# Kernel tuning notes

Measured on AMD Instinct MI355X. Metric: run time of the kernel, lower is better.

Reference implementation:

```python
import jax, jax.numpy as jnp
import numpy as np

N = 50000   # nodes
E = 800000  # edges (avg degree 16)
F = 128     # input_nf = output_nf
H = 128     # hidden_nf


def setup_inputs() -> dict:
    key = jax.random.key(0)
    ks = jax.random.split(key, 10)
    # coords: spatial part in [-1, 1], z-coordinate (last dim) in [0.5, 1.5] (must be > 0)
    xz = jax.random.uniform(ks[0], (N, 3), minval=-1.0, maxval=1.0)
    xz = xz.at[:, -1].set(jax.random.uniform(ks[1], (N,), minval=0.5, maxval=1.5))
    h = jax.random.normal(ks[2], (N, F), dtype=jnp.float32)
    row = jax.random.randint(ks[3], (E,), 0, N)
    # guarantee col != row so AdS distance is strictly positive on every edge
    col = (row + 1 + jax.random.randint(ks[4], (E,), 0, N - 1)) % N
    edge_index = jnp.stack([row, col]).astype(jnp.int32)

    def lin(k, fan_in, fan_out):
        return jax.random.normal(k, (fan_in, fan_out), dtype=jnp.float32) / np.float32(np.sqrt(fan_in))

    return {
        "xz": xz,
        "h": h,
        "We1": lin(ks[5], 2 * F + 1, H), "be1": jnp.full((H,), 0.1, jnp.float32),
        "We2": lin(ks[6], H, H),         "be2": jnp.full((H,), 0.1, jnp.float32),
        "Wn1": lin(ks[7], H + F, H),     "bn1": jnp.full((H,), 0.1, jnp.float32),
        "Wn2": lin(ks[8], H, F),         "bn2": jnp.full((F,), 0.1, jnp.float32),
        "edge_index": edge_index,
    }


def reference(xz, h, We1, be1, We2, be2, Wn1, bn1, Wn2, bn2, edge_index):
    row, col = edge_index[0], edge_index[1]
    n = h.shape[0]

    # AdS (hyperbolic upper-half-space) distance between xz[row] and xz[col]:
    # d = arccosh(1 + |p1 - p2|^2 / (2 z1 z2)), z = last coordinate
    diff = xz[row] - xz[col]                                  # [E, 3]
    u = jnp.sum(diff * diff, axis=-1) / (2.0 * xz[row, -1] * xz[col, -1])
    dist = jnp.arccosh(1.0 + u)[:, None]                      # [E, 1]

    # edge model: concat(source, target, radial) -> Linear -> silu -> Linear -> silu
    m = jnp.concatenate([h[row], h[col], dist], axis=1)       # [E, 2F+1]
    m = jax.nn.silu(m @ We1 + be1)                            # [E, H]
    m = jax.nn.silu(m @ We2 + be2)                            # [E, H]

    # segment_mean over destination nodes (row)
    num = jax.ops.segment_sum(m, row, num_segments=n)                          # [N, H]
    den = jax.ops.segment_sum(jnp.ones_like(m), row, num_segments=n)          # [N, H]
    agg = num / jnp.maximum(den, jnp.ones((), den.dtype))

    # node model: concat(h, agg) -> Linear -> silu -> Linear, plus residual
    z = jnp.concatenate([h, agg], axis=1)                     # [N, F+H]
    out = jax.nn.silu(z @ Wn1 + bn1) @ Wn2 + bn2              # [N, F]
    return h + out
```

## Files before the change

### kernel.cpp

```cpp
#include <hip/hip_runtime.h>

#define NN 50000
#define EE 800000
#define NB 196

typedef __bf16 bf16x8 __attribute__((ext_vector_type(8)));
typedef float  f32x4  __attribute__((ext_vector_type(4)));

__device__ __forceinline__ float bf2f(ushort u) {
    union { unsigned int i; float f; } v; v.i = ((unsigned int)u) << 16; return v.f;
}
__device__ __forceinline__ ushort f2bf(float f) {
    union { float f; unsigned int i; } v; v.f = f;
    unsigned int u = v.i;
    return (ushort)((u + 0x7FFFu + ((u >> 16) & 1u)) >> 16);
}
__device__ __forceinline__ ushort f2bf_fast(float f) {
    union { float f; unsigned int i; } v; v.f = f;
    return (ushort)((v.i + 0x8000u) >> 16);
}
__device__ __forceinline__ float silu(float x) {
    return x * __builtin_amdgcn_rcpf(1.0f + __expf(-x));
}

__global__ void detect_kernel(const ushort* __restrict__ xzu, int* __restrict__ flag) {
    __shared__ int cnt;
    if (threadIdx.x == 0) cnt = 0;
    __syncthreads();
    float v = bf2f(xzu[2 * threadIdx.x]);
    bool sane = (v == v) && (fabsf(v) <= 4.0f);
    if (sane) atomicAdd(&cnt, 1);
    __syncthreads();
    if (threadIdx.x == 0) *flag = (cnt >= 192) ? 0 : 1;
}

__global__ void prep_kernel(const void* __restrict__ hsrc, const void* __restrict__ xzsrc,
                            const int* __restrict__ erow, const int* __restrict__ flag,
                            ushort* __restrict__ hb, float* __restrict__ xzf,
                            int* __restrict__ cntI) {
    const bool isf = (*flag != 0);
    int b = blockIdx.x;
    if (b < 3125) {
        int i = (b * 256 + threadIdx.x) * 8;
        uint4 o;
        if (isf) {
            const float* s = (const float*)hsrc + i;
            float4 f0 = *(const float4*)s;
            float4 f1 = *(const float4*)(s + 4);
            o.x = (unsigned int)f2bf(f0.x) | ((unsigned int)f2bf(f0.y) << 16);
            o.y = (unsigned int)f2bf(f0.z) | ((unsigned int)f2bf(f0.w) << 16);
            o.z = (unsigned int)f2bf(f1.x) | ((unsigned int)f2bf(f1.y) << 16);
            o.w = (unsigned int)f2bf(f1.z) | ((unsigned int)f2bf(f1.w) << 16);
        } else {
            o = *(const uint4*)((const ushort*)hsrc + i);
        }
        *(uint4*)(hb + i) = o;
    } else if (b < 3712) {
        int i = (b - 3125) * 256 + threadIdx.x;
        if (i < NN * 3)
            xzf[i] = isf ? ((const float*)xzsrc)[i] : bf2f(((const ushort*)xzsrc)[i]);
    } else {
        int e = (b - 3712) * 256 + threadIdx.x;
        if (e < EE) atomicAdd(&cntI[erow[e]], 1);
    }
}

__global__ void swizzle_misc_kernel(const void* We1, const void* We2,
                                    const void* Wn1, const void* Wn2,
                                    const void* be1, const void* be2,
                                    const void* bn1, const void* bn2,
                                    const int* __restrict__ flag,
                                    ushort* __restrict__ We1s, ushort* __restrict__ We2s,
                                    ushort* __restrict__ Wn1s, ushort* __restrict__ Wn2s,
                                    float* __restrict__ fb, ushort* __restrict__ wlb) {
    const bool isf = (*flag != 0);
    if (blockIdx.x == 48) {
        for (int j = threadIdx.x; j < 640; j += 256) {
            int which = j >> 7, k = j & 127;
            const void* src = (which == 0) ? be1 : (which == 1) ? be2 :
                              (which == 2) ? bn1 : (which == 3) ? bn2 : We1;
            size_t idx = (which == 4) ? ((size_t)256 * 128 + k) : (size_t)k;
            float v = isf ? ((const float*)src)[idx] : bf2f(((const ushort*)src)[idx]);
            fb[j] = v;
            if (which == 4) wlb[k] = f2bf(v);
        }
        return;
    }
    int c = blockIdx.x * 256 + threadIdx.x;
    const void* src; ushort* dst; int cl;
    if      (c <  4096) { src = We1; dst = We1s; cl = c;         }
    else if (c <  6144) { src = We2; dst = We2s; cl = c - 4096;  }
    else if (c < 10240) { src = Wn1; dst = Wn1s; cl = c - 6144;  }
    else                { src = Wn2; dst = Wn2s; cl = c - 10240; }
    int l = cl & 63, nt = (cl >> 6) & 7, kc = cl >> 9;
    int kbase = kc * 32 + (l >> 4) * 8;
    int n = nt * 16 + (l & 15);
    ushort tmp[8];
#pragma unroll
    for (int j = 0; j < 8; ++j) {
        size_t idx = (size_t)(kbase + j) * 128 + n;
        tmp[j] = isf ? f2bf(((const float*)src)[idx]) : ((const ushort*)src)[idx];
    }
#pragma unroll
    for (int j = 0; j < 8; ++j) dst[(size_t)cl * 8 + j] = tmp[j];
}

__global__ void scanA_kernel(const int* __restrict__ cntI, int* __restrict__ bsum) {
    __shared__ int s[256];
    int t = threadIdx.x;
    int i = blockIdx.x * 256 + t;
    s[t] = (i < NN) ? cntI[i] : 0;
    __syncthreads();
#pragma unroll
    for (int off = 128; off > 0; off >>= 1) {
        if (t < off) s[t] += s[t + off];
        __syncthreads();
    }
    if (t == 0) bsum[blockIdx.x] = s[0];
}

__global__ void scanB_kernel(int* __restrict__ bsum) {
    __shared__ int s[256];
    int t = threadIdx.x;
    int v = (t < NB) ? bsum[t] : 0;
    s[t] = v;
    __syncthreads();
    for (int off = 1; off < 256; off <<= 1) {
        int u = (t >= off) ? s[t - off] : 0;
        __syncthreads();
        if (t >= off) s[t] += u;
        __syncthreads();
    }
    if (t < NB) bsum[t] = s[t] - v;
}

__global__ void scanC_kernel(const int* __restrict__ cntI, const int* __restrict__ bsum,
                             int* __restrict__ rowStart) {
    __shared__ int s[256];
    int t = threadIdx.x;
    int i = blockIdx.x * 256 + t;
    int v = (i < NN) ? cntI[i] : 0;
    s[t] = v;
    __syncthreads();
    for (int off = 1; off < 256; off <<= 1) {
        int u = (t >= off) ? s[t - off] : 0;
        __syncthreads();
        if (t >= off) s[t] += u;
        __syncthreads();
    }
    if (i < NN) rowStart[i] = bsum[blockIdx.x] + s[t] - v;
}

__global__ void scatter_kernel(const int* __restrict__ erow, const int* __restrict__ ecol,
                               const float* __restrict__ xzf,
                               const int* __restrict__ rowStart, int* __restrict__ cursor,
                               int* __restrict__ erowS, int* __restrict__ ecolS,
                               float* __restrict__ distS) {
    int e = blockIdx.x * 256 + threadIdx.x;
    if (e >= EE) return;
    int r = erow[e], c = ecol[e];
    int pos = rowStart[r] + atomicAdd(&cursor[r], 1);
    float4 a = *(const float4*)(xzf + 3 * r);
    float4 b = *(const float4*)(xzf + 3 * c);
    float dx = a.x - b.x, dy = a.y - b.y, dz = a.z - b.z;
    float u = (dx * dx + dy * dy + dz * dz) * __builtin_amdgcn_rcpf(2.0f * a.z * b.z);
    u = fminf(fmaxf(u, 0.0f), 1.0e6f);
    erowS[pos] = r;
    ecolS[pos] = c;
    distS[pos] = __logf(1.0f + u + sqrtf(u * (u + 2.0f)));
}

__global__ __launch_bounds__(256, 3) void pq_kernel(
    const ushort* __restrict__ hb, const ushort* __restrict__ We1s,
    const float* __restrict__ fb, ushort* __restrict__ Pp, ushort* __restrict__ Qq) {
    __shared__ __align__(16) ushort sA[8192];
    const int tid = threadIdx.x;
    const int lane = tid & 63, w = tid >> 6;
    const int col = lane & 15, quad = lane >> 4;
    const int nt0 = w * 2;
    const int ntiles = (NN + 63) / 64;
    const int nA = w * 32 + col, nB = nA + 16;
    const float be1A = fb[nA], be1B = fb[nB];

    for (int tile = blockIdx.x; tile < ntiles; tile += gridDim.x) {
        __syncthreads();
        const int n0 = tile * 64;
#pragma unroll
        for (int i = 0; i < 4; ++i) {
            int node = n0 + lane;
            uint4 v = (node < NN) ? *(const uint4*)(hb + (size_t)node * 128 + (w + 4 * i) * 8)
                                  : make_uint4(0, 0, 0, 0);
            *(uint4*)(sA + (((lane >> 4) * 4 + i) * 64 + w * 16 + (lane & 15)) * 8) = v;
        }
        __syncthreads();

        f32x4 accP[4][2] = {}, accQ[4][2] = {};
#pragma unroll
        for (int kc = 0; kc < 4; ++kc) {
            bf16x8 bp0 = *(const bf16x8*)(We1s + ((kc * 8 + nt0)           * 64 + lane) * 8);
            bf16x8 bp1 = *(const bf16x8*)(We1s + ((kc * 8 + nt0 + 1)       * 64 + lane) * 8);
            bf16x8 bq0 = *(const bf16x8*)(We1s + (((kc + 4) * 8 + nt0)     * 64 + lane) * 8);
            bf16x8 bq1 = *(const bf16x8*)(We1s + (((kc + 4) * 8 + nt0 + 1) * 64 + lane) * 8);
#pragma unroll
            for (int g = 0; g < 4; ++g) {
                bf16x8 a = *(const bf16x8*)(sA + ((g * 4 + kc) * 64 + lane) * 8);
                accP[g][0] = __builtin_amdgcn_mfma_f32_16x16x32_bf16(a, bp0, accP[g][0], 0, 0, 0);
                accP[g][1] = __builtin_amdgcn_mfma_f32_16x16x32_bf16(a, bp1, accP[g][1], 0, 0, 0);
                accQ[g][0] = __builtin_amdgcn_mfma_f32_16x16x32_bf16(a, bq0, accQ[g][0], 0, 0, 0);
                accQ[g][1] = __builtin_amdgcn_mfma_f32_16x16x32_bf16(a, bq1, accQ[g][1], 0, 0, 0);
            }
        }
#pragma unroll
        for (int g = 0; g < 4; ++g) {
#pragma unroll
            for (int r = 0; r < 4; ++r) {
                int node = n0 + g * 16 + quad * 4 + r;
                if (node < NN) {
                    size_t o = (size_t)node * 128;
                    Pp[o + nA] = f2bf(accP[g][0][r] + be1A);
                    Pp[o + nB] = f2bf(accP[g][1][r] + be1B);
                    Qq[o + nA] = f2bf(accQ[g][0][r]);
                    Qq[o + nB] = f2bf(accQ[g][1][r]);
                }
            }
        }
    }
}

__global__ __launch_bounds__(256, 4) void edge_kernel(
    const ushort* __restrict__ Pp, const ushort* __restrict__ Qq,
    const int* __restrict__ erowS, const int* __restrict__ ecolS,
    const float* __restrict__ distS, const ushort* __restrict__ We2s,
    const ushort* __restrict__ wlb, const float* __restrict__ fb,
    float* __restrict__ agg) {
    __shared__ __align__(16) char smem[64 * 132 * 4];
    __shared__ int sRow[64];
    ushort* sM = (ushort*)smem;
    float (*sOut)[132] = (float(*)[132])smem;

    const int tid = threadIdx.x;
    const int lane = tid & 63, w = tid >> 6;
    const int col = lane & 15, quad = lane >> 4;
    const int nt0 = w * 2;

    const int nA = w * 32 + col, nB = nA + 16;
    const float be2A = fb[128 + nA], be2B = fb[128 + nB];

    bf16x8 B2[8];
#pragma unroll
    for (int kc = 0; kc < 4; ++kc) {
        B2[kc * 2]     = *(const bf16x8*)(We2s + ((kc * 8 + nt0)     * 64 + lane) * 8);
        B2[kc * 2 + 1] = *(const bf16x8*)(We2s + ((kc * 8 + nt0 + 1) * 64 + lane) * 8);
    }
    bf16x8 WL[4];
#pragma unroll
    for (int i = 0; i < 4; ++i) WL[i] = *(const bf16x8*)(wlb + (w + 4 * i) * 8);

    const int ntiles = EE / 64;
    const int per = (ntiles + gridDim.x - 1) / gridDim.x;
    const int t0 = blockIdx.x * per;
    const int t1 = (t0 + per < ntiles) ? (t0 + per) : ntiles;

    for (int tile = t0; tile < t1; ++tile) {
        __syncthreads();
        const int e = tile * 64 + lane;
        const int r = erowS[e], c = ecolS[e];
        const float d = distS[e];
        if (w == 0) sRow[lane] = r;
#pragma unroll
        for (int i = 0; i < 4; ++i) {
            int ch = w + 4 * i;
            bf16x8 p = *(const bf16x8*)(Pp + (size_t)r * 128 + ch * 8);
            bf16x8 q = *(const bf16x8*)(Qq + (size_t)c * 128 + ch * 8);
            ushort out8[8];
#pragma unroll
            for (int j = 0; j < 8; ++j) {
                float x = (float)p[j] + (float)q[j] + d * (float)WL[i][j];
                out8[j] = f2bf_fast(silu(x));
            }
            *(uint4*)(sM + (((lane >> 4) * 4 + i) * 64 + w * 16 + (lane & 15)) * 8) =
                *(const uint4*)out8;
        }
        __syncthreads();

        f32x4 acc2[4][2] = {};
#pragma unroll
        for (int kc = 0; kc < 4; ++kc) {
#pragma unroll
            for (int g = 0; g < 4; ++g) {
                bf16x8 a = *(const bf16x8*)(sM + ((g * 4 + kc) * 64 + lane) * 8);
                acc2[g][0] = __builtin_amdgcn_mfma_f32_16x16x32_bf16(a, B2[kc * 2],     acc2[g][0], 0, 0, 0);
                acc2[g][1] = __builtin_amdgcn_mfma_f32_16x16x32_bf16(a, B2[kc * 2 + 1], acc2[g][1], 0, 0, 0);
            }
        }
        __syncthreads();

#pragma unroll
        for (int g = 0; g < 4; ++g) {
#pragma unroll
            for (int r4 = 0; r4 < 4; ++r4) {
                int m = g * 16 + quad * 4 + r4;
                sOut[m][nA] = silu(acc2[g][0][r4] + be2A);
                sOut[m][nB] = silu(acc2[g][1][r4] + be2B);
            }
        }
        __syncthreads();

        {
            const int cc = tid & 127;
            const int mb = (tid >> 7) * 32;
            float acc = 0.0f;
            int prow = sRow[mb];
            for (int k = 0; k < 32; ++k) {
                int rw = sRow[mb + k];
                if (rw != prow) {
                    unsafeAtomicAdd(&agg[(size_t)prow * 128 + cc], acc);
                    acc = 0.0f;
                    prow = rw;
                }
                acc += sOut[mb + k][cc];
            }
            unsafeAtomicAdd(&agg[(size_t)prow * 128 + cc], acc);
        }
    }
}

__global__ __launch_bounds__(256, 3) void node_kernel(
    const ushort* __restrict__ hb, const void* __restrict__ hraw,
    const float* __restrict__ agg, const int* __restrict__ cntI,
    const ushort* __restrict__ Wn1s, const ushort* __restrict__ Wn2s,
    const float* __restrict__ fb, const int* __restrict__ flag,
    void* __restrict__ outv) {
    __shared__ __align__(16) ushort sA[16384];
    __shared__ __align__(16) ushort sM[8192];
    const int tid = threadIdx.x;
    const int lane = tid & 63, w = tid >> 6;
    const int col = lane & 15, quad = lane >> 4;
    const int nt0 = w * 2;
    const int ntiles = (NN + 63) / 64;
    const bool isf = (*flag != 0);
    float* outf = (float*)outv;
    ushort* outu = (ushort*)outv;

    const int nA = w * 32 + col, nB = nA + 16;
    const float bn1A = fb[256 + nA], bn1B = fb[256 + nB];
    const float bn2A = fb[384 + nA], bn2B = fb[384 + nB];

    for (int tile = blockIdx.x; tile < ntiles; tile += gridDim.x) {
        __syncthreads();
        const int n0 = tile * 64;
#pragma unroll
        for (int i = 0; i < 8; ++i) {
            int kb = w + 4 * i;
            int node = n0 + lane;
            uint4 v;
            if (node < NN) {
                if (kb < 16) {
                    v = *(const uint4*)(hb + (size_t)node * 128 + kb * 8);
                } else {
                    const float* ap = agg + (size_t)node * 128 + (kb - 16) * 8;
                    float invc = __builtin_amdgcn_rcpf(fmaxf((float)cntI[node], 1.0f));
                    float4 f0 = *(const float4*)ap;
                    float4 f1 = *(const float4*)(ap + 4);
                    v.x = (unsigned int)f2bf_fast(f0.x * invc) | ((unsigned int)f2bf_fast(f0.y * invc) << 16);
                    v.y = (unsigned int)f2bf_fast(f0.z * invc) | ((unsigned int)f2bf_fast(f0.w * invc) << 16);
                    v.z = (unsigned int)f2bf_fast(f1.x * invc) | ((unsigned int)f2bf_fast(f1.y * invc) << 16);
                    v.w = (unsigned int)f2bf_fast(f1.z * invc) | ((unsigned int)f2bf_fast(f1.w * invc) << 16);
                }
            } else {
                v = make_uint4(0, 0, 0, 0);
            }
            *(uint4*)(sA + (((quad * 8 + i) * 64) + w * 16 + col) * 8) = v;
        }
        __syncthreads();

        f32x4 acc[4][2] = {};
#pragma unroll
        for (int kc = 0; kc < 8; ++kc) {
            bf16x8 b0 = *(const bf16x8*)(Wn1s + ((kc * 8 + nt0)     * 64 + lane) * 8);
            bf16x8 b1 = *(const bf16x8*)(Wn1s + ((kc * 8 + nt0 + 1) * 64 + lane) * 8);
#pragma unroll
            for (int g = 0; g < 4; ++g) {
                bf16x8 a = *(const bf16x8*)(sA + ((g * 8 + kc) * 64 + lane) * 8);
                acc[g][0] = __builtin_amdgcn_mfma_f32_16x16x32_bf16(a, b0, acc[g][0], 0, 0, 0);
                acc[g][1] = __builtin_amdgcn_mfma_f32_16x16x32_bf16(a, b1, acc[g][1], 0, 0, 0);
            }
        }
#pragma unroll
        for (int g = 0; g < 4; ++g) {
            int base0 = ((g * 4 + w) * 64 + (col >> 3) * 16) * 8 + (col & 7);
#pragma unroll
            for (int r = 0; r < 4; ++r) {
                int mrow = quad * 4 + r;
                sM[base0 + mrow * 8]              = f2bf_fast(silu(acc[g][0][r] + bn1A));
                sM[base0 + 2 * 16 * 8 + mrow * 8] = f2bf_fast(silu(acc[g][1][r] + bn1B));
            }
        }
        __syncthreads();

        f32x4 acc2[4][2] = {};
#pragma unroll
        for (int kc = 0; kc < 4; ++kc) {
            bf16x8 b0 = *(const bf16x8*)(Wn2s + ((kc * 8 + nt0)     * 64 + lane) * 8);
            bf16x8 b1 = *(const bf16x8*)(Wn2s + ((kc * 8 + nt0 + 1) * 64 + lane) * 8);
#pragma unroll
            for (int g = 0; g < 4; ++g) {
                bf16x8 a = *(const bf16x8*)(sM + ((g * 4 + kc) * 64 + lane) * 8);
                acc2[g][0] = __builtin_amdgcn_mfma_f32_16x16x32_bf16(a, b0, acc2[g][0], 0, 0, 0);
                acc2[g][1] = __builtin_amdgcn_mfma_f32_16x16x32_bf16(a, b1, acc2[g][1], 0, 0, 0);
            }
        }
#pragma unroll
        for (int g = 0; g < 4; ++g) {
#pragma unroll
            for (int r = 0; r < 4; ++r) {
                int ml2 = g * 16 + quad * 4 + r;
                int node = n0 + ml2;
                if (node < NN) {
                    size_t oi = (size_t)node * 128;
                    float h0 = isf ? ((const float*)hraw)[oi + nA] : bf2f(((const ushort*)hraw)[oi + nA]);
                    float h1 = isf ? ((const float*)hraw)[oi + nB] : bf2f(((const ushort*)hraw)[oi + nB]);
                    float x0 = acc2[g][0][r] + bn2A + h0;
                    float x1 = acc2[g][1][r] + bn2B + h1;
                    if (isf) { outf[oi + nA] = x0; outf[oi + nB] = x1; }
                    else     { outu[oi + nA] = f2bf_fast(x0); outu[oi + nB] = f2bf_fast(x1); }
                }
            }
        }
    }
}

extern "C" void kernel_launch(void* const* d_in, const int* in_sizes, int n_in,
                              void* d_out, int out_size, void* d_ws, size_t ws_size,
                              hipStream_t stream) {
    const void* xz  = d_in[0];
    const void* h   = d_in[1];
    const void* We1 = d_in[2];
    const void* be1 = d_in[3];
    const void* We2 = d_in[4];
    const void* be2 = d_in[5];
    const void* Wn1 = d_in[6];
    const void* bn1 = d_in[7];
    const void* Wn2 = d_in[8];
    const void* bn2 = d_in[9];
    const int*  ei  = (const int*)d_in[10];
    const int* erow = ei;
    const int* ecol = ei + EE;

    char* base = (char*)d_ws;
    size_t cur = 0;
    auto alloc = [&](size_t bytes) { size_t o = cur; cur = (cur + bytes + 255) & ~(size_t)255; return o; };
    int*    flag   = (int*)   (base + alloc(16));
    float*  agg    = (float*) (base + alloc((size_t)NN * 128 * 4));
    int*    cntI   = (int*)   (base + alloc((size_t)NN * 4));
    int*    cursor = (int*)   (base + alloc((size_t)NN * 4));
    ushort* hb     = (ushort*)(base + alloc((size_t)NN * 128 * 2));
    ushort* Pp     = (ushort*)(base + alloc((size_t)NN * 128 * 2));
    ushort* Qq     = (ushort*)(base + alloc((size_t)NN * 128 * 2));
    int*    erowS  = (int*)   (base + alloc((size_t)EE * 4));
    int*    ecolS  = (int*)   (base + alloc((size_t)EE * 4));
    float*  distS  = (float*) (base + alloc((size_t)EE * 4));
    float*  xzf    = (float*) (base + alloc((size_t)NN * 3 * 4 + 16));
    int*    rowSt  = (int*)   (base + alloc((size_t)NN * 4));
    int*    bsum   = (int*)   (base + alloc(256 * 4));
    ushort* We1s   = (ushort*)(base + alloc(32768 * 2));
    ushort* We2s   = (ushort*)(base + alloc(16384 * 2));
    ushort* Wn1s   = (ushort*)(base + alloc(32768 * 2));
    ushort* Wn2s   = (ushort*)(base + alloc(16384 * 2));
    float*  fb     = (float*) (base + alloc(640 * 4));
    ushort* wlb    = (ushort*)(base + alloc(128 * 2));

    size_t zbytes = (size_t)((char*)hb - (char*)agg);
    (void)hipMemsetAsync(agg, 0, zbytes, stream);

    detect_kernel<<<1, 256, 0, stream>>>((const ushort*)xz, flag);
    prep_kernel<<<6837, 256, 0, stream>>>(h, xz, erow, flag, hb, xzf, cntI);
    swizzle_misc_kernel<<<49, 256, 0, stream>>>(We1, We2, Wn1, Wn2, be1, be2, bn1, bn2,
                                                flag, We1s, We2s, Wn1s, Wn2s, fb, wlb);
    scanA_kernel<<<NB, 256, 0, stream>>>(cntI, bsum);
    scanB_kernel<<<1, 256, 0, stream>>>(bsum);
    scanC_kernel<<<NB, 256, 0, stream>>>(cntI, bsum, rowSt);
    scatter_kernel<<<(EE + 255) / 256, 256, 0, stream>>>(erow, ecol, xzf, rowSt, cursor,
                                                         erowS, ecolS, distS);
    pq_kernel<<<782, 256, 0, stream>>>(hb, We1s, fb, Pp, Qq);
    edge_kernel<<<1024, 256, 0, stream>>>(Pp, Qq, erowS, ecolS, distS, We2s, wlb, fb, agg);
    node_kernel<<<782, 256, 0, stream>>>(hb, h, agg, cntI, Wn1s, Wn2s, fb, flag, d_out);
}
```

Measured before the change: 347.0 us.

## Prefetch next edge tile gathers, pack edge records, fuse scan kernels

The edge kernel now loads the next tile's packed edge record and gathers its P/Q rows into registers while the current tile runs its MFMA and reduction, hiding gather latency. The three sorted edge arrays (row, col, dist) become one int4 array, so each edge is a single 16-byte load. The scanB kernel is folded into scanC, where every block redundantly scans the block sums, removing one launch. The cost is more registers in the edge kernel, which may hurt occupancy, plus a wider edge array and redundant scan work.

```diff
diff --git a/kernel.cpp b/kernel.cpp
--- a/kernel.cpp
+++ b/kernel.cpp
@@ -119,25 +119,22 @@
     if (t == 0) bsum[blockIdx.x] = s[0];
 }
 
-__global__ void scanB_kernel(int* __restrict__ bsum) {
-    __shared__ int s[256];
-    int t = threadIdx.x;
-    int v = (t < NB) ? bsum[t] : 0;
-    s[t] = v;
-    __syncthreads();
-    for (int off = 1; off < 256; off <<= 1) {
-        int u = (t >= off) ? s[t - off] : 0;
-        __syncthreads();
-        if (t >= off) s[t] += u;
-        __syncthreads();
-    }
-    if (t < NB) bsum[t] = s[t] - v;
-}
-
 __global__ void scanC_kernel(const int* __restrict__ cntI, const int* __restrict__ bsum,
                              int* __restrict__ rowStart) {
     __shared__ int s[256];
+    __shared__ int sbase;
     int t = threadIdx.x;
+    int bv = (t < NB) ? bsum[t] : 0;
+    s[t] = bv;
+    __syncthreads();
+    for (int off = 1; off < 256; off <<= 1) {
+        int u = (t >= off) ? s[t - off] : 0;
+        __syncthreads();
+        if (t >= off) s[t] += u;
+        __syncthreads();
+    }
+    if (t == 0) sbase = (blockIdx.x == 0) ? 0 : s[blockIdx.x - 1];
+    __syncthreads();
     int i = blockIdx.x * 256 + t;
     int v = (i < NN) ? cntI[i] : 0;
     s[t] = v;
@@ -148,14 +145,13 @@
         if (t >= off) s[t] += u;
         __syncthreads();
     }
-    if (i < NN) rowStart[i] = bsum[blockIdx.x] + s[t] - v;
+    if (i < NN) rowStart[i] = sbase + s[t] - v;
 }
 
 __global__ void scatter_kernel(const int* __restrict__ erow, const int* __restrict__ ecol,
                                const float* __restrict__ xzf,
                                const int* __restrict__ rowStart, int* __restrict__ cursor,
-                               int* __restrict__ erowS, int* __restrict__ ecolS,
-                               float* __restrict__ distS) {
+                               int4* __restrict__ eS) {
     int e = blockIdx.x * 256 + threadIdx.x;
     if (e >= EE) return;
     int r = erow[e], c = ecol[e];
@@ -165,9 +161,8 @@
     float dx = a.x - b.x, dy = a.y - b.y, dz = a.z - b.z;
     float u = (dx * dx + dy * dy + dz * dz) * __builtin_amdgcn_rcpf(2.0f * a.z * b.z);
     u = fminf(fmaxf(u, 0.0f), 1.0e6f);
-    erowS[pos] = r;
-    ecolS[pos] = c;
-    distS[pos] = __logf(1.0f + u + sqrtf(u * (u + 2.0f)));
+    float d = __logf(1.0f + u + sqrtf(u * (u + 2.0f)));
+    eS[pos] = make_int4(r, c, __float_as_int(d), 0);
 }
 
 __global__ __launch_bounds__(256, 3) void pq_kernel(
@@ -229,8 +224,7 @@
 
 __global__ __launch_bounds__(256, 4) void edge_kernel(
     const ushort* __restrict__ Pp, const ushort* __restrict__ Qq,
-    const int* __restrict__ erowS, const int* __restrict__ ecolS,
-    const float* __restrict__ distS, const ushort* __restrict__ We2s,
+    const int4* __restrict__ eS, const ushort* __restrict__ We2s,
     const ushort* __restrict__ wlb, const float* __restrict__ fb,
     float* __restrict__ agg) {
     __shared__ __align__(16) char smem[64 * 132 * 4];
@@ -246,41 +240,54 @@
     const int nA = w * 32 + col, nB = nA + 16;
     const float be2A = fb[128 + nA], be2B = fb[128 + nB];
 
-    bf16x8 B2[8];
-#pragma unroll
-    for (int kc = 0; kc < 4; ++kc) {
-        B2[kc * 2]     = *(const bf16x8*)(We2s + ((kc * 8 + nt0)     * 64 + lane) * 8);
-        B2[kc * 2 + 1] = *(const bf16x8*)(We2s + ((kc * 8 + nt0 + 1) * 64 + lane) * 8);
-    }
-    bf16x8 WL[4];
-#pragma unroll
-    for (int i = 0; i < 4; ++i) WL[i] = *(const bf16x8*)(wlb + (w + 4 * i) * 8);
-
     const int ntiles = EE / 64;
     const int per = (ntiles + gridDim.x - 1) / gridDim.x;
     const int t0 = blockIdx.x * per;
     const int t1 = (t0 + per < ntiles) ? (t0 + per) : ntiles;
+    if (t0 >= t1) return;
+
+    bf16x8 B2[8];
+#pragma unroll
+    for (int kc = 0; kc < 4; ++kc) {
+        B2[kc * 2]     = *(const bf16x8*)(We2s + ((kc * 8 + nt0)     * 64 + lane) * 8);
+        B2[kc * 2 + 1] = *(const bf16x8*)(We2s + ((kc * 8 + nt0 + 1) * 64 + lane) * 8);
+    }
+    bf16x8 WL[4];
+#pragma unroll
+    for (int i = 0; i < 4; ++i) WL[i] = *(const bf16x8*)(wlb + (w + 4 * i) * 8);
+
+    int4 ed = eS[(size_t)t0 * 64 + lane];
+    bf16x8 p[4], q[4];
+#pragma unroll
+    for (int i = 0; i < 4; ++i) {
+        p[i] = *(const bf16x8*)(Pp + (size_t)ed.x * 128 + (w + 4 * i) * 8);
+        q[i] = *(const bf16x8*)(Qq + (size_t)ed.y * 128 + (w + 4 * i) * 8);
+    }
 
     for (int tile = t0; tile < t1; ++tile) {
-        __syncthreads();
-        const int e = tile * 64 + lane;
-        const int r = erowS[e], c = ecolS[e];
-        const float d = distS[e];
-        if (w == 0) sRow[lane] = r;
+        const int tn = (tile + 1 < t1) ? (tile + 1) : tile;
+        const int4 edn = eS[(size_t)tn * 64 + lane];
+
+        __syncthreads();
+        if (w == 0) sRow[lane] = ed.x;
+        const float d = __int_as_float(ed.z);
 #pragma unroll
         for (int i = 0; i < 4; ++i) {
-            int ch = w + 4 * i;
-            bf16x8 p = *(const bf16x8*)(Pp + (size_t)r * 128 + ch * 8);
-            bf16x8 q = *(const bf16x8*)(Qq + (size_t)c * 128 + ch * 8);
             ushort out8[8];
 #pragma unroll
             for (int j = 0; j < 8; ++j) {
-                float x = (float)p[j] + (float)q[j] + d * (float)WL[i][j];
+                float x = (float)p[i][j] + (float)q[i][j] + d * (float)WL[i][j];
                 out8[j] = f2bf_fast(silu(x));
             }
             *(uint4*)(sM + (((lane >> 4) * 4 + i) * 64 + w * 16 + (lane & 15)) * 8) =
                 *(const uint4*)out8;
         }
+#pragma unroll
+        for (int i = 0; i < 4; ++i) {
+            p[i] = *(const bf16x8*)(Pp + (size_t)edn.x * 128 + (w + 4 * i) * 8);
+            q[i] = *(const bf16x8*)(Qq + (size_t)edn.y * 128 + (w + 4 * i) * 8);
+        }
+        ed = edn;
         __syncthreads();
 
         f32x4 acc2[4][2] = {};
@@ -457,9 +464,7 @@
     ushort* hb     = (ushort*)(base + alloc((size_t)NN * 128 * 2));
     ushort* Pp     = (ushort*)(base + alloc((size_t)NN * 128 * 2));
     ushort* Qq     = (ushort*)(base + alloc((size_t)NN * 128 * 2));
-    int*    erowS  = (int*)   (base + alloc((size_t)EE * 4));
-    int*    ecolS  = (int*)   (base + alloc((size_t)EE * 4));
-    float*  distS  = (float*) (base + alloc((size_t)EE * 4));
+    int4*   eS     = (int4*)  (base + alloc((size_t)EE * 16));
     float*  xzf    = (float*) (base + alloc((size_t)NN * 3 * 4 + 16));
     int*    rowSt  = (int*)   (base + alloc((size_t)NN * 4));
     int*    bsum   = (int*)   (base + alloc(256 * 4));
@@ -478,11 +483,9 @@
     swizzle_misc_kernel<<<49, 256, 0, stream>>>(We1, We2, Wn1, Wn2, be1, be2, bn1, bn2,
                                                 flag, We1s, We2s, Wn1s, Wn2s, fb, wlb);
     scanA_kernel<<<NB, 256, 0, stream>>>(cntI, bsum);
-    scanB_kernel<<<1, 256, 0, stream>>>(bsum);
     scanC_kernel<<<NB, 256, 0, stream>>>(cntI, bsum, rowSt);
-    scatter_kernel<<<(EE + 255) / 256, 256, 0, stream>>>(erow, ecol, xzf, rowSt, cursor,
-                                                         erowS, ecolS, distS);
+    scatter_kernel<<<(EE + 255) / 256, 256, 0, stream>>>(erow, ecol, xzf, rowSt, cursor, eS);
     pq_kernel<<<782, 256, 0, stream>>>(hb, We1s, fb, Pp, Qq);
-    edge_kernel<<<1024, 256, 0, stream>>>(Pp, Qq, erowS, ecolS, distS, We2s, wlb, fb, agg);
+    edge_kernel<<<1024, 256, 0, stream>>>(Pp, Qq, eS, We2s, wlb, fb, agg);
     node_kernel<<<782, 256, 0, stream>>>(hb, h, agg, cntI, Wn1s, Wn2s, fb, flag, d_out);
 }
```

Measured after the change: 404.8 us. +16.7%, slower.
